# Kernel tuning notes

Hardware: AMD Instinct MI355X
Metric: run time of the kernel (lower is better)

The kernel has to match this reference:

```python
import jax, jax.numpy as jnp
import numpy as np
import math

B, M, DM = 8, 512, 1024
H, DH = 16, 64
DFF = 4096
RA, RF, RO = 32, 384, 384
EPS = 1e-12  # BERT LayerNorm eps


def layernorm(x, g, b):
    mu = jnp.mean(x, axis=-1, keepdims=True)
    var = jnp.mean(jnp.square(x - mu), axis=-1, keepdims=True)
    return (x - mu) * jax.lax.rsqrt(var + EPS) * g + b


def setup_inputs() -> dict:
    key = jax.random.key(0)
    ks = jax.random.split(key, 24)
    s = 0.02
    inp = {
        "x": jax.random.normal(ks[0], (B, M, DM), jnp.float32),
        "mask": jnp.zeros((B, M), jnp.float32),  # additive attention mask
        "Pq": jax.random.normal(ks[1], (H, DM, RA), jnp.float32) * s,
        "Vq": jax.random.normal(ks[2], (H, RA, DH), jnp.float32) * s,
        "Pk": jax.random.normal(ks[3], (H, DM, RA), jnp.float32) * s,
        "Vk": jax.random.normal(ks[4], (H, RA, DH), jnp.float32) * s,
        "Pv": jax.random.normal(ks[5], (H, DM, RA), jnp.float32) * s,
        "Vv": jax.random.normal(ks[6], (H, RA, DH), jnp.float32) * s,
        "bq": jax.random.normal(ks[7], (H, DH), jnp.float32) * s,
        "bk": jax.random.normal(ks[8], (H, DH), jnp.float32) * s,
        "bv": jax.random.normal(ks[9], (H, DH), jnp.float32) * s,
        "Uo": jax.random.normal(ks[10], (DM, RO), jnp.float32) * s,
        "Vo": jax.random.normal(ks[11], (RO, DM), jnp.float32) * s,
        "bo_attn": jax.random.normal(ks[12], (DM,), jnp.float32) * s,
        "U1": jax.random.normal(ks[13], (DM, RF), jnp.float32) * s,
        "V1": jax.random.normal(ks[14], (RF, DFF), jnp.float32) * s,
        "b1": jax.random.normal(ks[15], (DFF,), jnp.float32) * s,
        "U2": jax.random.normal(ks[16], (DFF, RF), jnp.float32) * s,
        "V2": jax.random.normal(ks[17], (RF, DM), jnp.float32) * s,
        "b2": jax.random.normal(ks[18], (DM,), jnp.float32) * s,
        "ln1_g": jnp.ones((DM,), jnp.float32),
        "ln1_b": jnp.zeros((DM,), jnp.float32),
        "ln2_g": jnp.ones((DM,), jnp.float32),
        "ln2_b": jnp.zeros((DM,), jnp.float32),
    }
    return inp


def reference(x, mask, Pq, Vq, Pk, Vk, Pv, Vv, bq, bk, bv,
              Uo, Vo, bo_attn, U1, V1, b1, U2, V2, b2,
              ln1_g, ln1_b, ln2_g, ln2_b):
    b_, m_, dm = x.shape
    h = Pq.shape[0]
    dh = dm // h
    # low-rank per-head projections: x -> [B,H,M,R] -> [B,H,M,dh]
    q = jnp.einsum('bmd,hdr->bhmr', x, Pq)
    k = jnp.einsum('bmd,hdr->bhmr', x, Pk)
    v = jnp.einsum('bmd,hdr->bhmr', x, Pv)
    Q = jnp.einsum('bhmr,hrd->bhmd', q, Vq) + bq[None, :, None, :]
    K = jnp.einsum('bhmr,hrd->bhmd', k, Vk) + bk[None, :, None, :]
    V = jnp.einsum('bhmr,hrd->bhmd', v, Vv) + bv[None, :, None, :]
    # scaled dot-product attention (flash_svd_attention equivalent)
    scores = jnp.einsum('bhmd,bhnd->bhmn', Q, K) / math.sqrt(dh)
    scores = scores + mask[:, None, None, :]
    probs = jax.nn.softmax(scores, axis=-1)
    attn = jnp.einsum('bhmn,bhnd->bhmd', probs, V)  # [B,H,M,dh]
    attn = attn.transpose(0, 2, 1, 3).reshape(b_, m_, dm)
    # low-rank output projection + residual + LN
    x1 = layernorm(x + (attn @ Uo) @ Vo + bo_attn, ln1_g, ln1_b)
    # flashsvd_ffn_v1 equivalent: gelu((x1 @ U1) @ V1 + b1) @ U2 @ V2 + b2
    mid = x1 @ U1
    hdn = jax.nn.gelu(mid @ V1 + b1, approximate=False)
    y = (hdn @ U2) @ V2 + b2
    out = layernorm(x1 + y, ln2_g, ln2_b)
    return out
```

## Files before the change

### kernel.cpp

```cpp
#include <hip/hip_runtime.h>
#include <math.h>

typedef __attribute__((ext_vector_type(8))) short short8;
typedef __attribute__((ext_vector_type(4))) float floatx4;

__device__ inline unsigned short f2bf(float f){
    union { float f; unsigned u; } v; v.f = f;
    unsigned r = v.u + 0x7fffu + ((v.u >> 16) & 1u);
    return (unsigned short)(r >> 16);
}
__device__ inline float bf2f(unsigned short b){
    union { unsigned u; float f; } v; v.u = ((unsigned)b) << 16;
    return v.f;
}
__device__ inline unsigned short to_bf(float f){ return f2bf(f); }
__device__ inline unsigned short to_bf(unsigned short u){ return u; }

#define GLD_LDS16(g, l) __builtin_amdgcn_global_load_lds( \
    (const __attribute__((address_space(1))) void*)(g),   \
    (__attribute__((address_space(3))) void*)(l), 16, 0, 0)

__global__ __launch_bounds__(256) void cast_kernel(const float* __restrict__ s,
                                                   unsigned short* __restrict__ d){
    int i = (blockIdx.x*256 + threadIdx.x)*4;
    float4 v = *(const float4*)(s+i);
    ushort4 o; o.x=f2bf(v.x); o.y=f2bf(v.y); o.z=f2bf(v.z); o.w=f2bf(v.w);
    *(ushort4*)(d+i) = o;
}

__global__ __launch_bounds__(256) void castP_kernel(
    const float* __restrict__ p0, const float* __restrict__ p1,
    const float* __restrict__ p2, unsigned short* __restrict__ d){
    int blk = blockIdx.x;
    int proj = blk >> 9;
    const float* s = (proj==0)?p0:(proj==1)?p1:p2;
    int off = (blk & 511)*1024 + threadIdx.x*4;
    float4 v = *(const float4*)(s+off);
    ushort4 o; o.x=f2bf(v.x); o.y=f2bf(v.y); o.z=f2bf(v.z); o.w=f2bf(v.w);
    *(ushort4*)(d + (size_t)proj*524288 + off) = o;
}

__global__ __launch_bounds__(256) void reduce4_kernel(
    const float* __restrict__ p, unsigned short* __restrict__ o, long mn){
    long i = ((long)blockIdx.x*256 + threadIdx.x)*4;
    float4 a = *(const float4*)(p+i);
    float4 b = *(const float4*)(p+mn+i);
    float4 c = *(const float4*)(p+2*mn+i);
    float4 d = *(const float4*)(p+3*mn+i);
    ushort4 r;
    r.x = f2bf(a.x+b.x+c.x+d.x); r.y = f2bf(a.y+b.y+c.y+d.y);
    r.z = f2bf(a.z+b.z+c.z+d.z); r.w = f2bf(a.w+b.w+c.w+d.w);
    *(ushort4*)(o+i) = r;
}

__global__ __launch_bounds__(256) void bcat_kernel(
    const float* __restrict__ bq, const float* __restrict__ bk,
    const float* __restrict__ bv, float* __restrict__ bcat){
    int i = blockIdx.x*256 + threadIdx.x;
    const float* p = (i < 1024) ? bq : (i < 2048) ? bk : bv;
    bcat[i] = p[i & 1023];
}

template<typename T>
__global__ __launch_bounds__(256) void trans_kernel(
    const T* __restrict__ src, unsigned short* __restrict__ dst,
    int R, int C, long sz, long dz)
{
    __shared__ unsigned short tile[32][33];
    const T* s = src + (size_t)blockIdx.z * sz;
    unsigned short* d = dst + (size_t)blockIdx.z * dz;
    int c0 = blockIdx.x*32, r0 = blockIdx.y*32;
    int tr = threadIdx.x>>3, tc = (threadIdx.x&7)*4;
    const T* sp = s + (size_t)(r0+tr)*C + c0 + tc;
#pragma unroll
    for (int i=0;i<4;i++) tile[tr][tc+i] = to_bf(sp[i]);
    __syncthreads();
    ushort4 o; o.x = tile[tc+0][tr]; o.y = tile[tc+1][tr];
    o.z = tile[tc+2][tr]; o.w = tile[tc+3][tr];
    *(ushort4*)(d + (size_t)(c0+tr)*R + r0 + tc) = o;
}

__global__ __launch_bounds__(256) void trans2_kernel(
    const float* __restrict__ s0, unsigned short* __restrict__ d0,
    const float* __restrict__ s1, unsigned short* __restrict__ d1,
    int R, int C)
{
    __shared__ unsigned short tile[32][33];
    const float* s = blockIdx.z ? s1 : s0;
    unsigned short* d = blockIdx.z ? d1 : d0;
    int c0 = blockIdx.x*32, r0 = blockIdx.y*32;
    int tr = threadIdx.x>>3, tc = (threadIdx.x&7)*4;
    const float* sp = s + (size_t)(r0+tr)*C + c0 + tc;
#pragma unroll
    for (int i=0;i<4;i++) tile[tr][tc+i] = f2bf(sp[i]);
    __syncthreads();
    ushort4 o; o.x = tile[tc+0][tr]; o.y = tile[tc+1][tr];
    o.z = tile[tc+2][tr]; o.w = tile[tc+3][tr];
    *(ushort4*)(d + (size_t)(c0+tr)*R + r0 + tc) = o;
}

__global__ __launch_bounds__(256) void vtrans3_kernel(
    const float* __restrict__ v0, const float* __restrict__ v1,
    const float* __restrict__ v2, unsigned short* __restrict__ dst)
{
    __shared__ unsigned short tile[32][33];
    int z = blockIdx.z;
    int proj = z >> 4, h = z & 15;
    const float* s = ((proj==0)?v0:(proj==1)?v1:v2) + h*2048;
    unsigned short* d = dst + (size_t)proj*32768 + h*2048;
    int c0 = blockIdx.x*32;
    int tr = threadIdx.x>>3, tc = (threadIdx.x&7)*4;
    const float* sp = s + (size_t)tr*64 + c0 + tc;
#pragma unroll
    for (int i=0;i<4;i++) tile[tr][tc+i] = f2bf(sp[i]);
    __syncthreads();
    ushort4 o; o.x = tile[tc+0][tr]; o.y = tile[tc+1][tr];
    o.z = tile[tc+2][tr]; o.w = tile[tc+3][tr];
    *(ushort4*)(d + (size_t)(c0+tr)*32 + tc) = o;
}

__global__ __launch_bounds__(256) void mm64_kernel(
    const unsigned short* __restrict__ A, const unsigned short* __restrict__ Bt,
    unsigned short* __restrict__ C, int Kdim, int lda, int ldb, int ldc,
    long ah, long al, long bh, long bl, long ch, long cl)
{
    __shared__ unsigned short As[64*40];
    __shared__ unsigned short Bs[64*40];
    int z = blockIdx.z;
    const unsigned short* Ab = A + (size_t)(z>>4)*ah + (size_t)(z&15)*al;
    const unsigned short* Bb = Bt + (size_t)(z>>4)*bh + (size_t)(z&15)*bl;
    int row0 = blockIdx.y*64, col0 = blockIdx.x*64;
    int t = threadIdx.x;
    int ar = t>>2, ak = (t&3)*8;
    int w = t>>6, lane = t&63, quad = lane>>4, c16 = lane&15;
    int wm = (w&1)*32, wn = (w>>1)*32;

    floatx4 zero = {0.f,0.f,0.f,0.f};
    floatx4 acc[2][2];
    acc[0][0]=zero; acc[0][1]=zero; acc[1][0]=zero; acc[1][1]=zero;

    const unsigned short* Ap = Ab + (size_t)(row0+ar)*lda + ak;
    const unsigned short* Bp = Bb + (size_t)(col0+ar)*ldb + ak;

    for (int kk=0; kk<Kdim; kk+=32){
        uint4 av = *(const uint4*)(Ap + kk);
        uint4 bv = *(const uint4*)(Bp + kk);
        __syncthreads();
        *(uint4*)(As + ar*40 + ak) = av;
        *(uint4*)(Bs + ar*40 + ak) = bv;
        __syncthreads();
        short8 a0 = *(const short8*)(As + (wm   +c16)*40 + quad*8);
        short8 a1 = *(const short8*)(As + (wm+16+c16)*40 + quad*8);
        short8 b0 = *(const short8*)(Bs + (wn   +c16)*40 + quad*8);
        short8 b1 = *(const short8*)(Bs + (wn+16+c16)*40 + quad*8);
        acc[0][0] = __builtin_amdgcn_mfma_f32_16x16x32_bf16(a0,b0,acc[0][0],0,0,0);
        acc[0][1] = __builtin_amdgcn_mfma_f32_16x16x32_bf16(a0,b1,acc[0][1],0,0,0);
        acc[1][0] = __builtin_amdgcn_mfma_f32_16x16x32_bf16(a1,b0,acc[1][0],0,0,0);
        acc[1][1] = __builtin_amdgcn_mfma_f32_16x16x32_bf16(a1,b1,acc[1][1],0,0,0);
    }

    size_t zc = (size_t)(z>>4)*ch + (size_t)(z&15)*cl;
#pragma unroll
    for (int mt=0; mt<2; mt++)
#pragma unroll
    for (int r=0; r<4; r++){
        int row = row0 + wm + mt*16 + quad*4 + r;
#pragma unroll
        for (int nt=0; nt<2; nt++){
            int col = col0 + wn + nt*16 + c16;
            C[zc + (size_t)row*ldc + col] = f2bf(acc[mt][nt][r]);
        }
    }
}

template<int EPI>
__global__ __launch_bounds__(256) void mm128_kernel(
    const unsigned short* __restrict__ A, const unsigned short* __restrict__ Bt,
    void* __restrict__ C, int Kdim, int lda, int ldb, int ldc,
    const float* __restrict__ aux, const float* __restrict__ resid)
{
    __shared__ unsigned short As[128*64];
    __shared__ unsigned short Bs[128*64];
    int row0 = blockIdx.y*128, col0 = blockIdx.x*128;
    int t = threadIdx.x;
    int w = t>>6, lane = t&63, quad = lane>>4, c16 = lane&15;
    int wm = (w&1)*64, wn = (w>>1)*64;

    int srow = lane>>3;
    int kc = (lane&7) ^ srow;
    const unsigned short* Ag = A + (size_t)(row0 + w*32 + srow)*lda + kc*8;
    const unsigned short* Bg = Bt + (size_t)(col0 + w*32 + srow)*ldb + kc*8;
    unsigned short* AsW = As + (w*32)*64;
    unsigned short* BsW = Bs + (w*32)*64;

    floatx4 acc[4][4];
#pragma unroll
    for (int i=0;i<4;i++)
#pragma unroll
    for (int j=0;j<4;j++) acc[i][j] = (floatx4){0.f,0.f,0.f,0.f};

    int xa = (c16&7)*8;

    for (int kk=0; kk<Kdim; kk+=64){
#pragma unroll
        for (int i=0;i<4;i++){
            GLD_LDS16(Ag + (size_t)(i*8)*lda + kk, AsW + i*512);
            GLD_LDS16(Bg + (size_t)(i*8)*ldb + kk, BsW + i*512);
        }
        __syncthreads();
#pragma unroll
        for (int ks=0; ks<2; ks++){
            short8 a[4], b[4];
#pragma unroll
            for (int mt=0; mt<4; mt++)
                a[mt] = *(const short8*)(As + (wm + mt*16 + c16)*64
                                            + (((ks*4 + quad)*8) ^ xa));
#pragma unroll
            for (int nt=0; nt<4; nt++)
                b[nt] = *(const short8*)(Bs + (wn + nt*16 + c16)*64
                                            + (((ks*4 + quad)*8) ^ xa));
#pragma unroll
            for (int mt=0; mt<4; mt++)
#pragma unroll
                for (int nt=0; nt<4; nt++)
                    acc[mt][nt] = __builtin_amdgcn_mfma_f32_16x16x32_bf16(
                        a[mt], b[nt], acc[mt][nt], 0,0,0);
        }
        __syncthreads();
    }

#pragma unroll
    for (int mt=0; mt<4; mt++)
#pragma unroll
    for (int r=0; r<4; r++){
        int row = row0 + wm + mt*16 + quad*4 + r;
#pragma unroll
        for (int nt=0; nt<4; nt++){
            int col = col0 + wn + nt*16 + c16;
            float v = acc[mt][nt][r];
            if (EPI==0) {
                ((unsigned short*)C)[(size_t)row*ldc + col] = f2bf(v);
            } else if (EPI==2) {
                v += aux[col];
                v = 0.5f*v*(1.0f + erff(v*0.70710678118654752f));
                ((unsigned short*)C)[(size_t)row*ldc + col] = f2bf(v);
            } else if (EPI==3) {
                ((float*)C)[(size_t)row*ldc + col] =
                    v + aux[col] + resid[(size_t)row*ldc + col];
            } else {
                int proj = col >> 10, cw = col & 1023;
                int b_ = row >> 9, m_ = row & 511;
                int hh = cw >> 6, dd = cw & 63;
                float vv = v + aux[col];
                if (proj == 0) vv *= 0.125f;
                size_t idx;
                if (proj == 2)
                    idx = (size_t)2*4194304 + ((size_t)(b_*16+hh)*64 + dd)*512 + m_;
                else
                    idx = (size_t)proj*4194304 + ((size_t)(b_*16+hh)*512 + m_)*64 + dd;
                ((unsigned short*)C)[idx] = f2bf(vv);
            }
        }
    }
}

__global__ __launch_bounds__(256) void mmsk_kernel(
    const unsigned short* __restrict__ A, const unsigned short* __restrict__ Bt,
    float* __restrict__ Cp, int Kchunk, int lda, int ldb, int ldc, long mn)
{
    __shared__ unsigned short As[128*64];
    __shared__ unsigned short Bs[128*64];
    int row0 = blockIdx.y*128, col0 = blockIdx.x*128;
    int t = threadIdx.x;
    int w = t>>6, lane = t&63, quad = lane>>4, c16 = lane&15;
    int wm = (w&1)*64, wn = (w>>1)*64;

    int srow = lane>>3;
    int kc = (lane&7) ^ srow;
    const unsigned short* Ag = A + (size_t)(row0 + w*32 + srow)*lda + kc*8;
    const unsigned short* Bg = Bt + (size_t)(col0 + w*32 + srow)*ldb + kc*8;
    unsigned short* AsW = As + (w*32)*64;
    unsigned short* BsW = Bs + (w*32)*64;

    floatx4 acc[4][4];
#pragma unroll
    for (int i=0;i<4;i++)
#pragma unroll
    for (int j=0;j<4;j++) acc[i][j] = (floatx4){0.f,0.f,0.f,0.f};

    int xa = (c16&7)*8;
    int k0 = blockIdx.z * Kchunk;
    for (int kk=k0; kk<k0+Kchunk; kk+=64){
#pragma unroll
        for (int i=0;i<4;i++){
            GLD_LDS16(Ag + (size_t)(i*8)*lda + kk, AsW + i*512);
            GLD_LDS16(Bg + (size_t)(i*8)*ldb + kk, BsW + i*512);
        }
        __syncthreads();
#pragma unroll
        for (int ks=0; ks<2; ks++){
            short8 a[4], b[4];
#pragma unroll
            for (int mt=0; mt<4; mt++)
                a[mt] = *(const short8*)(As + (wm + mt*16 + c16)*64
                                            + (((ks*4 + quad)*8) ^ xa));
#pragma unroll
            for (int nt=0; nt<4; nt++)
                b[nt] = *(const short8*)(Bs + (wn + nt*16 + c16)*64
                                            + (((ks*4 + quad)*8) ^ xa));
#pragma unroll
            for (int mt=0; mt<4; mt++)
#pragma unroll
                for (int nt=0; nt<4; nt++)
                    acc[mt][nt] = __builtin_amdgcn_mfma_f32_16x16x32_bf16(
                        a[mt], b[nt], acc[mt][nt], 0,0,0);
        }
        __syncthreads();
    }

    float* Cz = Cp + (size_t)blockIdx.z * mn;
#pragma unroll
    for (int mt=0; mt<4; mt++)
#pragma unroll
    for (int r=0; r<4; r++){
        int row = row0 + wm + mt*16 + quad*4 + r;
#pragma unroll
        for (int nt=0; nt<4; nt++){
            int col = col0 + wn + nt*16 + c16;
            Cz[(size_t)row*ldc + col] = acc[mt][nt][r];
        }
    }
}

__global__ __launch_bounds__(256) void flash_kernel(
    const unsigned short* __restrict__ Qb, const unsigned short* __restrict__ Kb,
    const unsigned short* __restrict__ Vt, const float* __restrict__ mask,
    unsigned short* __restrict__ attn)
{
    __shared__ unsigned short Ks[64*64];
    __shared__ unsigned short Vts[64*64];
    __shared__ unsigned short Ps[4][16*64];

    int qt = blockIdx.x, bh = blockIdx.y;
    int b = bh >> 4, h = bh & 15;
    int t = threadIdx.x;
    int w = t>>6, lane = t&63, quad = lane>>4, c16 = lane&15;

    int qrow = qt*64 + w*16 + c16;
    const unsigned short* Qp = Qb + ((size_t)bh*512 + qrow)*64 + quad*8;
    short8 qf0 = *(const short8*)(Qp);
    short8 qf1 = *(const short8*)(Qp + 32);

    const unsigned short* Ktile0 = Kb + (size_t)bh*512*64;
    const unsigned short* Vtbh = Vt + (size_t)bh*32768;

    int srow = lane>>3;
    int kc = (lane&7) ^ srow;
    int xa = (c16&7)*8;

    floatx4 Oacc[4];
#pragma unroll
    for (int nd=0;nd<4;nd++) Oacc[nd] = (floatx4){0.f,0.f,0.f,0.f};
    float mrow[4], lrow[4];
#pragma unroll
    for (int r=0;r<4;r++){ mrow[r] = -3.0e38f; lrow[r] = 0.f; }

    unsigned short* Pw = &Ps[w][0];

    for (int kt=0; kt<8; kt++){
        __syncthreads();
#pragma unroll
        for (int i=0;i<2;i++){
            GLD_LDS16(Ktile0 + (size_t)(kt*64 + w*16 + i*8 + srow)*64 + kc*8,
                      Ks + (w*16+i*8)*64);
            GLD_LDS16(Vtbh + (size_t)(w*16 + i*8 + srow)*512 + kt*64 + kc*8,
                      Vts + (w*16+i*8)*64);
        }
        __syncthreads();

        floatx4 Sacc[4];
#pragma unroll
        for (int nt=0;nt<4;nt++){
            float mv = mask[b*512 + kt*64 + nt*16 + c16];
            Sacc[nt] = (floatx4){mv,mv,mv,mv};
        }
#pragma unroll
        for (int ks=0; ks<2; ks++){
            short8 qk = ks ? qf1 : qf0;
            short8 bfr[4];
#pragma unroll
            for (int nt=0;nt<4;nt++)
                bfr[nt] = *(const short8*)(Ks + (nt*16 + c16)*64
                                              + (((ks*4 + quad)*8) ^ xa));
#pragma unroll
            for (int nt=0;nt<4;nt++)
                Sacc[nt] = __builtin_amdgcn_mfma_f32_16x16x32_bf16(
                    qk, bfr[nt], Sacc[nt], 0,0,0);
        }

#pragma unroll
        for (int r=0;r<4;r++){
            float sv0 = Sacc[0][r], sv1 = Sacc[1][r],
                  sv2 = Sacc[2][r], sv3 = Sacc[3][r];
            float rmax = fmaxf(fmaxf(sv0,sv1), fmaxf(sv2,sv3));
            rmax = fmaxf(rmax, __shfl_xor(rmax, 1));
            rmax = fmaxf(rmax, __shfl_xor(rmax, 2));
            rmax = fmaxf(rmax, __shfl_xor(rmax, 4));
            rmax = fmaxf(rmax, __shfl_xor(rmax, 8));
            float mold = mrow[r];
            float mnew = fmaxf(mold, rmax);
            float alpha = __expf(mold - mnew);
            float p0 = __expf(sv0-mnew), p1 = __expf(sv1-mnew);
            float p2 = __expf(sv2-mnew), p3 = __expf(sv3-mnew);
            float ps = p0+p1+p2+p3;
            ps += __shfl_xor(ps, 1);
            ps += __shfl_xor(ps, 2);
            ps += __shfl_xor(ps, 4);
            ps += __shfl_xor(ps, 8);
            lrow[r] = lrow[r]*alpha + ps;
            mrow[r] = mnew;
#pragma unroll
            for (int nd=0;nd<4;nd++) Oacc[nd][r] *= alpha;
            int rl = quad*4 + r;
            int rx = rl & 7;
            int cb = rl*64 + (c16&7);
            Pw[cb + (((0*2 + (c16>>3)) ^ rx)*8)] = f2bf(p0);
            Pw[cb + (((1*2 + (c16>>3)) ^ rx)*8)] = f2bf(p1);
            Pw[cb + (((2*2 + (c16>>3)) ^ rx)*8)] = f2bf(p2);
            Pw[cb + (((3*2 + (c16>>3)) ^ rx)*8)] = f2bf(p3);
        }

#pragma unroll
        for (int ks=0; ks<2; ks++){
            short8 pa = *(const short8*)(Pw + c16*64 + (((ks*4 + quad)*8) ^ xa));
            short8 bfr[4];
#pragma unroll
            for (int nd=0;nd<4;nd++)
                bfr[nd] = *(const short8*)(Vts + (nd*16 + c16)*64
                                               + (((ks*4 + quad)*8) ^ xa));
#pragma unroll
            for (int nd=0;nd<4;nd++)
                Oacc[nd] = __builtin_amdgcn_mfma_f32_16x16x32_bf16(
                    pa, bfr[nd], Oacc[nd], 0,0,0);
        }
    }

#pragma unroll
    for (int r=0;r<4;r++){
        int m = qt*64 + w*16 + quad*4 + r;
        float inv = 1.0f / lrow[r];
        unsigned short* op = attn + ((size_t)(b*512 + m))*1024 + h*64;
#pragma unroll
        for (int nd=0;nd<4;nd++)
            op[nd*16 + c16] = f2bf(Oacc[nd][r] * inv);
    }
}

template<int DUAL>
__global__ __launch_bounds__(256) void ln_kernel(
    const float* __restrict__ in, const float* __restrict__ g,
    const float* __restrict__ bta, float* __restrict__ outf,
    unsigned short* __restrict__ outb)
{
    int row = blockIdx.x;
    int t = threadIdx.x;
    const float* x = in + (size_t)row*1024;
    float4 xv = ((const float4*)x)[t];
    float s  = xv.x + xv.y + xv.z + xv.w;
    float ss = xv.x*xv.x + xv.y*xv.y + xv.z*xv.z + xv.w*xv.w;
#pragma unroll
    for (int off=32; off>0; off>>=1){ s += __shfl_down(s, off); ss += __shfl_down(ss, off); }
    __shared__ float rs[4], rss[4];
    int wid = t>>6, lane = t&63;
    if (lane==0){ rs[wid]=s; rss[wid]=ss; }
    __syncthreads();
    s  = rs[0]+rs[1]+rs[2]+rs[3];
    ss = rss[0]+rss[1]+rss[2]+rss[3];
    float mu  = s * (1.0f/1024.0f);
    float var = ss * (1.0f/1024.0f) - mu*mu;
    float inv = rsqrtf(var + 1e-12f);
    float4 gv = ((const float4*)g)[t];
    float4 bv = ((const float4*)bta)[t];
    float4 o = make_float4((xv.x-mu)*inv*gv.x+bv.x, (xv.y-mu)*inv*gv.y+bv.y,
                           (xv.z-mu)*inv*gv.z+bv.z, (xv.w-mu)*inv*gv.w+bv.w);
    ((float4*)(outf + (size_t)row*1024))[t] = o;
    if (DUAL){
        ushort4 ob; ob.x=f2bf(o.x); ob.y=f2bf(o.y); ob.z=f2bf(o.z); ob.w=f2bf(o.w);
        ((ushort4*)(outb + (size_t)row*1024))[t] = ob;
    }
}

extern "C" void kernel_launch(void* const* d_in, const int* in_sizes, int n_in,
                              void* d_out, int out_size, void* d_ws, size_t ws_size,
                              hipStream_t stream)
{
    const float* x       = (const float*)d_in[0];
    const float* mask    = (const float*)d_in[1];
    const float* Pq      = (const float*)d_in[2];
    const float* Vq      = (const float*)d_in[3];
    const float* Pk      = (const float*)d_in[4];
    const float* Vk      = (const float*)d_in[5];
    const float* Pv      = (const float*)d_in[6];
    const float* Vv      = (const float*)d_in[7];
    const float* bq      = (const float*)d_in[8];
    const float* bk      = (const float*)d_in[9];
    const float* bv      = (const float*)d_in[10];
    const float* Uo      = (const float*)d_in[11];
    const float* Vo      = (const float*)d_in[12];
    const float* bo_attn = (const float*)d_in[13];
    const float* U1      = (const float*)d_in[14];
    const float* V1      = (const float*)d_in[15];
    const float* b1      = (const float*)d_in[16];
    const float* U2      = (const float*)d_in[17];
    const float* V2      = (const float*)d_in[18];
    const float* b2      = (const float*)d_in[19];
    const float* ln1_g   = (const float*)d_in[20];
    const float* ln1_b   = (const float*)d_in[21];
    const float* ln2_g   = (const float*)d_in[22];
    const float* ln2_b   = (const float*)d_in[23];
    float* out = (float*)d_out;

    char* base = (char*)d_ws;
    unsigned short* Uo_t   = (unsigned short*)(base + 0);
    unsigned short* Vo_t   = (unsigned short*)(base + 786432);
    unsigned short* U1_t   = (unsigned short*)(base + 1572864);
    unsigned short* V1_t   = (unsigned short*)(base + 2359296);
    unsigned short* U2_t   = (unsigned short*)(base + 5505024);
    unsigned short* V2_t   = (unsigned short*)(base + 8650752);
    float*          bcat   = (float*)(base + 9437184);
    unsigned short* Wt     = (unsigned short*)(base + 9449472);
    unsigned short* Pbf    = (unsigned short*)(base + 15740928);
    unsigned short* Vt2    = (unsigned short*)(base + 18886656);
    unsigned short* x_bf   = (unsigned short*)(base + 19083264);
    unsigned short* t_bf   = (unsigned short*)(base + 9449472);
    float*          ybuf   = (float*)(base + 12595200);
    float*          x1     = (float*)(base + 29372416);
    unsigned short* x1_bf  = (unsigned short*)(base + 46149632);
    unsigned short* hdn_bf = (unsigned short*)(base + 54538240);
    float*          part0  = (float*)(base + 12595200);
    float*          part1  = (float*)(base + 54538240);
    float*          part2  = (float*)(base + 88092672);
    unsigned short* Qb     = (unsigned short*)(base + 76558336);
    unsigned short* Kb     = (unsigned short*)(base + 84946944);
    unsigned short* Vt     = (unsigned short*)(base + 93535552);
    unsigned short* attn_bf= (unsigned short*)(base + 110312768);

    const long MN384 = 4096L*384;

    cast_kernel<<<4096,256,0,stream>>>(x, x_bf);
    castP_kernel<<<1536,256,0,stream>>>(Pq, Pk, Pv, Pbf);
    vtrans3_kernel<<<dim3(2,1,48),256,0,stream>>>(Vq, Vk, Vv, Vt2);
    bcat_kernel<<<12,256,0,stream>>>(bq, bk, bv, bcat);
    trans2_kernel<<<dim3(12,32,2),256,0,stream>>>(Uo, Uo_t, U1, U1_t, 1024, 384);
    trans2_kernel<<<dim3(32,12,2),256,0,stream>>>(Vo, Vo_t, V2, V2_t, 384, 1024);
    trans_kernel<float><<<dim3(128,12,1),256,0,stream>>>(V1, V1_t, 384,4096, 0,0);
    trans_kernel<float><<<dim3(12,128,1),256,0,stream>>>(U2, U2_t, 4096,384, 0,0);

    mm64_kernel<<<dim3(16,1,48),256,0,stream>>>(Vt2, Pbf, Wt,
        32, 32, 32, 1024, 32768,2048, 524288,32768, 1048576,65536);

    mm128_kernel<4><<<dim3(24,32,1),256,0,stream>>>(x_bf, Wt, Qb,
        1024, 1024, 1024, 3072, bcat, nullptr);

    flash_kernel<<<dim3(8,128),256,0,stream>>>(Qb, Kb, Vt, mask, attn_bf);

    mmsk_kernel<<<dim3(3,32,4),256,0,stream>>>(attn_bf, Uo_t, part0,
        256, 1024, 1024, 384, MN384);
    reduce4_kernel<<<1536,256,0,stream>>>(part0, t_bf, MN384);
    mm128_kernel<3><<<dim3(8,32,1),256,0,stream>>>(t_bf, Vo_t, ybuf,
        384, 384, 384, 1024, bo_attn, x);
    ln_kernel<1><<<4096,256,0,stream>>>(ybuf, ln1_g, ln1_b, x1, x1_bf);
    mmsk_kernel<<<dim3(3,32,4),256,0,stream>>>(x1_bf, U1_t, part1,
        256, 1024, 1024, 384, MN384);
    reduce4_kernel<<<1536,256,0,stream>>>(part1, t_bf, MN384);
    mm128_kernel<2><<<dim3(32,32,1),256,0,stream>>>(t_bf, V1_t, hdn_bf,
        384, 384, 384, 4096, b1, nullptr);
    mmsk_kernel<<<dim3(3,32,4),256,0,stream>>>(hdn_bf, U2_t, part2,
        1024, 4096, 4096, 384, MN384);
    reduce4_kernel<<<1536,256,0,stream>>>(part2, t_bf, MN384);
    mm128_kernel<3><<<dim3(8,32,1),256,0,stream>>>(t_bf, V2_t, ybuf,
        384, 384, 384, 1024, b2, x1);
    ln_kernel<0><<<4096,256,0,stream>>>(ybuf, ln2_g, ln2_b, out, nullptr);
}
```

Baseline: 375.2 us.

## Merge prep kernels, stage GEMM epilogues through LDS, store split-K partials as bf16

Folds the eight weight and input cast/transpose launches into one prep kernel that dispatches on block index, cutting launch overhead. The GEMM epilogues (QKV scatter, GELU output, split-K partials) now stage the tile in shared memory and write 16-byte coalesced rows instead of scattered 2-byte stores. Split-K partials are stored as bf16 instead of fp32, halving partial traffic and reduce4 reads, at the cost of extra rounding before the sum.

```diff
diff --git a/kernel.cpp b/kernel.cpp
--- a/kernel.cpp
+++ b/kernel.cpp
@@ -13,83 +13,15 @@
     union { unsigned u; float f; } v; v.u = ((unsigned)b) << 16;
     return v.f;
 }
-__device__ inline unsigned short to_bf(float f){ return f2bf(f); }
-__device__ inline unsigned short to_bf(unsigned short u){ return u; }
 
 #define GLD_LDS16(g, l) __builtin_amdgcn_global_load_lds( \
     (const __attribute__((address_space(1))) void*)(g),   \
     (__attribute__((address_space(3))) void*)(l), 16, 0, 0)
 
-__global__ __launch_bounds__(256) void cast_kernel(const float* __restrict__ s,
-                                                   unsigned short* __restrict__ d){
-    int i = (blockIdx.x*256 + threadIdx.x)*4;
-    float4 v = *(const float4*)(s+i);
-    ushort4 o; o.x=f2bf(v.x); o.y=f2bf(v.y); o.z=f2bf(v.z); o.w=f2bf(v.w);
-    *(ushort4*)(d+i) = o;
-}
-
-__global__ __launch_bounds__(256) void castP_kernel(
-    const float* __restrict__ p0, const float* __restrict__ p1,
-    const float* __restrict__ p2, unsigned short* __restrict__ d){
-    int blk = blockIdx.x;
-    int proj = blk >> 9;
-    const float* s = (proj==0)?p0:(proj==1)?p1:p2;
-    int off = (blk & 511)*1024 + threadIdx.x*4;
-    float4 v = *(const float4*)(s+off);
-    ushort4 o; o.x=f2bf(v.x); o.y=f2bf(v.y); o.z=f2bf(v.z); o.w=f2bf(v.w);
-    *(ushort4*)(d + (size_t)proj*524288 + off) = o;
-}
-
-__global__ __launch_bounds__(256) void reduce4_kernel(
-    const float* __restrict__ p, unsigned short* __restrict__ o, long mn){
-    long i = ((long)blockIdx.x*256 + threadIdx.x)*4;
-    float4 a = *(const float4*)(p+i);
-    float4 b = *(const float4*)(p+mn+i);
-    float4 c = *(const float4*)(p+2*mn+i);
-    float4 d = *(const float4*)(p+3*mn+i);
-    ushort4 r;
-    r.x = f2bf(a.x+b.x+c.x+d.x); r.y = f2bf(a.y+b.y+c.y+d.y);
-    r.z = f2bf(a.z+b.z+c.z+d.z); r.w = f2bf(a.w+b.w+c.w+d.w);
-    *(ushort4*)(o+i) = r;
-}
-
-__global__ __launch_bounds__(256) void bcat_kernel(
-    const float* __restrict__ bq, const float* __restrict__ bk,
-    const float* __restrict__ bv, float* __restrict__ bcat){
-    int i = blockIdx.x*256 + threadIdx.x;
-    const float* p = (i < 1024) ? bq : (i < 2048) ? bk : bv;
-    bcat[i] = p[i & 1023];
-}
-
-template<typename T>
-__global__ __launch_bounds__(256) void trans_kernel(
-    const T* __restrict__ src, unsigned short* __restrict__ dst,
-    int R, int C, long sz, long dz)
-{
-    __shared__ unsigned short tile[32][33];
-    const T* s = src + (size_t)blockIdx.z * sz;
-    unsigned short* d = dst + (size_t)blockIdx.z * dz;
-    int c0 = blockIdx.x*32, r0 = blockIdx.y*32;
-    int tr = threadIdx.x>>3, tc = (threadIdx.x&7)*4;
-    const T* sp = s + (size_t)(r0+tr)*C + c0 + tc;
-#pragma unroll
-    for (int i=0;i<4;i++) tile[tr][tc+i] = to_bf(sp[i]);
-    __syncthreads();
-    ushort4 o; o.x = tile[tc+0][tr]; o.y = tile[tc+1][tr];
-    o.z = tile[tc+2][tr]; o.w = tile[tc+3][tr];
-    *(ushort4*)(d + (size_t)(c0+tr)*R + r0 + tc) = o;
-}
-
-__global__ __launch_bounds__(256) void trans2_kernel(
-    const float* __restrict__ s0, unsigned short* __restrict__ d0,
-    const float* __restrict__ s1, unsigned short* __restrict__ d1,
-    int R, int C)
-{
-    __shared__ unsigned short tile[32][33];
-    const float* s = blockIdx.z ? s1 : s0;
-    unsigned short* d = blockIdx.z ? d1 : d0;
-    int c0 = blockIdx.x*32, r0 = blockIdx.y*32;
-    int tr = threadIdx.x>>3, tc = (threadIdx.x&7)*4;
+__device__ inline void tbody(const float* __restrict__ s,
+                             unsigned short* __restrict__ d, int R, int C,
+                             int c0, int r0, int t, unsigned short tile[][33]){
+    int tr = t>>3, tc = (t&7)*4;
     const float* sp = s + (size_t)(r0+tr)*C + c0 + tc;
 #pragma unroll
     for (int i=0;i<4;i++) tile[tr][tc+i] = f2bf(sp[i]);
@@ -99,24 +31,90 @@
     *(ushort4*)(d + (size_t)(c0+tr)*R + r0 + tc) = o;
 }
 
-__global__ __launch_bounds__(256) void vtrans3_kernel(
-    const float* __restrict__ v0, const float* __restrict__ v1,
-    const float* __restrict__ v2, unsigned short* __restrict__ dst)
+__global__ __launch_bounds__(256) void prep_kernel(
+    const float* __restrict__ x, unsigned short* __restrict__ x_bf,
+    const float* __restrict__ Pq, const float* __restrict__ Pk,
+    const float* __restrict__ Pv, unsigned short* __restrict__ Pbf,
+    const float* __restrict__ Vq, const float* __restrict__ Vk,
+    const float* __restrict__ Vv, unsigned short* __restrict__ Vt2,
+    const float* __restrict__ bq, const float* __restrict__ bk,
+    const float* __restrict__ bv, float* __restrict__ bcat,
+    const float* __restrict__ Uo, unsigned short* __restrict__ Uo_t,
+    const float* __restrict__ U1, unsigned short* __restrict__ U1_t,
+    const float* __restrict__ Vo, unsigned short* __restrict__ Vo_t,
+    const float* __restrict__ V2, unsigned short* __restrict__ V2_t,
+    const float* __restrict__ V1, unsigned short* __restrict__ V1_t,
+    const float* __restrict__ U2, unsigned short* __restrict__ U2_t)
 {
     __shared__ unsigned short tile[32][33];
-    int z = blockIdx.z;
-    int proj = z >> 4, h = z & 15;
-    const float* s = ((proj==0)?v0:(proj==1)?v1:v2) + h*2048;
-    unsigned short* d = dst + (size_t)proj*32768 + h*2048;
-    int c0 = blockIdx.x*32;
-    int tr = threadIdx.x>>3, tc = (threadIdx.x&7)*4;
-    const float* sp = s + (size_t)tr*64 + c0 + tc;
-#pragma unroll
-    for (int i=0;i<4;i++) tile[tr][tc+i] = f2bf(sp[i]);
-    __syncthreads();
-    ushort4 o; o.x = tile[tc+0][tr]; o.y = tile[tc+1][tr];
-    o.z = tile[tc+2][tr]; o.w = tile[tc+3][tr];
-    *(ushort4*)(d + (size_t)(c0+tr)*32 + tc) = o;
+    int bid = blockIdx.x, t = threadIdx.x;
+    if (bid < 4096){
+        int i = (bid*256 + t)*4;
+        float4 v = *(const float4*)(x+i);
+        ushort4 o; o.x=f2bf(v.x); o.y=f2bf(v.y); o.z=f2bf(v.z); o.w=f2bf(v.w);
+        *(ushort4*)(x_bf+i) = o;
+    } else if (bid < 5632){
+        int blk = bid - 4096;
+        int proj = blk >> 9;
+        const float* s = (proj==0)?Pq:(proj==1)?Pk:Pv;
+        int off = (blk & 511)*1024 + t*4;
+        float4 v = *(const float4*)(s+off);
+        ushort4 o; o.x=f2bf(v.x); o.y=f2bf(v.y); o.z=f2bf(v.z); o.w=f2bf(v.w);
+        *(ushort4*)(Pbf + (size_t)proj*524288 + off) = o;
+    } else if (bid < 5728){
+        int local = bid - 5632;
+        int gx = local & 1, z = local >> 1;
+        int proj = z >> 4, h = z & 15;
+        const float* s = ((proj==0)?Vq:(proj==1)?Vk:Vv) + h*2048;
+        unsigned short* d = Vt2 + (size_t)proj*32768 + h*2048;
+        int c0 = gx*32;
+        int tr = t>>3, tc = (t&7)*4;
+        const float* sp = s + (size_t)tr*64 + c0 + tc;
+#pragma unroll
+        for (int i=0;i<4;i++) tile[tr][tc+i] = f2bf(sp[i]);
+        __syncthreads();
+        ushort4 o; o.x = tile[tc+0][tr]; o.y = tile[tc+1][tr];
+        o.z = tile[tc+2][tr]; o.w = tile[tc+3][tr];
+        *(ushort4*)(d + (size_t)(c0+tr)*32 + tc) = o;
+    } else if (bid < 5740){
+        int i = (bid-5728)*256 + t;
+        const float* p = (i < 1024) ? bq : (i < 2048) ? bk : bv;
+        bcat[i] = p[i & 1023];
+    } else if (bid < 6508){
+        int local = bid - 5740;
+        const float* s = Uo; unsigned short* d = Uo_t;
+        if (local >= 384){ s = U1; d = U1_t; local -= 384; }
+        tbody(s, d, 1024, 384, (local%12)*32, (local/12)*32, t, tile);
+    } else if (bid < 7276){
+        int local = bid - 6508;
+        const float* s = Vo; unsigned short* d = Vo_t;
+        if (local >= 384){ s = V2; d = V2_t; local -= 384; }
+        tbody(s, d, 384, 1024, (local%32)*32, (local/32)*32, t, tile);
+    } else if (bid < 8812){
+        int local = bid - 7276;
+        tbody(V1, V1_t, 384, 4096, (local%128)*32, (local/128)*32, t, tile);
+    } else {
+        int local = bid - 8812;
+        tbody(U2, U2_t, 4096, 384, (local%12)*32, (local/12)*32, t, tile);
+    }
+}
+
+__global__ __launch_bounds__(256) void reduce4_kernel(
+    const unsigned short* __restrict__ p, unsigned short* __restrict__ o, long mn){
+    long i = ((long)blockIdx.x*256 + threadIdx.x)*8;
+    uint4 a = *(const uint4*)(p+i);
+    uint4 b = *(const uint4*)(p+mn+i);
+    uint4 c = *(const uint4*)(p+2*mn+i);
+    uint4 d = *(const uint4*)(p+3*mn+i);
+    const unsigned short* ua = (const unsigned short*)&a;
+    const unsigned short* ub = (const unsigned short*)&b;
+    const unsigned short* uc = (const unsigned short*)&c;
+    const unsigned short* ud = (const unsigned short*)&d;
+    uint4 r; unsigned short* ur = (unsigned short*)&r;
+#pragma unroll
+    for (int j=0;j<8;j++)
+        ur[j] = f2bf(bf2f(ua[j]) + bf2f(ub[j]) + bf2f(uc[j]) + bf2f(ud[j]));
+    *(uint4*)(o+i) = r;
 }
 
 __global__ __launch_bounds__(256) void mm64_kernel(
@@ -179,8 +177,9 @@
     void* __restrict__ C, int Kdim, int lda, int ldb, int ldc,
     const float* __restrict__ aux, const float* __restrict__ resid)
 {
-    __shared__ unsigned short As[128*64];
-    __shared__ unsigned short Bs[128*64];
+    __shared__ unsigned short smem[(EPI==3) ? 16384 : 17408];
+    unsigned short* As = smem;
+    unsigned short* Bs = smem + 8192;
     int row0 = blockIdx.y*128, col0 = blockIdx.x*128;
     int t = threadIdx.x;
     int w = t>>6, lane = t&63, quad = lane>>4, c16 = lane&15;
@@ -229,47 +228,76 @@
         __syncthreads();
     }
 
+    if (EPI==3){
+#pragma unroll
+        for (int mt=0; mt<4; mt++)
+#pragma unroll
+        for (int r=0; r<4; r++){
+            int row = row0 + wm + mt*16 + quad*4 + r;
+#pragma unroll
+            for (int nt=0; nt<4; nt++){
+                int col = col0 + wn + nt*16 + c16;
+                ((float*)C)[(size_t)row*ldc + col] =
+                    acc[mt][nt][r] + aux[col] + resid[(size_t)row*ldc + col];
+            }
+        }
+        return;
+    }
+
+    int proj = col0 >> 10;
 #pragma unroll
     for (int mt=0; mt<4; mt++)
 #pragma unroll
     for (int r=0; r<4; r++){
-        int row = row0 + wm + mt*16 + quad*4 + r;
+        int row_l = wm + mt*16 + quad*4 + r;
 #pragma unroll
         for (int nt=0; nt<4; nt++){
-            int col = col0 + wn + nt*16 + c16;
+            int col_l = wn + nt*16 + c16;
             float v = acc[mt][nt][r];
-            if (EPI==0) {
-                ((unsigned short*)C)[(size_t)row*ldc + col] = f2bf(v);
-            } else if (EPI==2) {
-                v += aux[col];
+            if (EPI==2){
+                v += aux[col0 + col_l];
                 v = 0.5f*v*(1.0f + erff(v*0.70710678118654752f));
-                ((unsigned short*)C)[(size_t)row*ldc + col] = f2bf(v);
-            } else if (EPI==3) {
-                ((float*)C)[(size_t)row*ldc + col] =
-                    v + aux[col] + resid[(size_t)row*ldc + col];
+                smem[row_l*136 + col_l] = f2bf(v);
             } else {
-                int proj = col >> 10, cw = col & 1023;
-                int b_ = row >> 9, m_ = row & 511;
-                int hh = cw >> 6, dd = cw & 63;
-                float vv = v + aux[col];
-                if (proj == 0) vv *= 0.125f;
-                size_t idx;
-                if (proj == 2)
-                    idx = (size_t)2*4194304 + ((size_t)(b_*16+hh)*64 + dd)*512 + m_;
-                else
-                    idx = (size_t)proj*4194304 + ((size_t)(b_*16+hh)*512 + m_)*64 + dd;
-                ((unsigned short*)C)[idx] = f2bf(vv);
+                v += aux[col0 + col_l];
+                if (proj == 0) v *= 0.125f;
+                if (proj < 2) smem[row_l*136 + col_l] = f2bf(v);
+                else          smem[col_l*136 + row_l] = f2bf(v);
             }
         }
+    }
+    __syncthreads();
+    int b_ = row0 >> 9;
+    int m0 = row0 & 511;
+    int cbase = col0 & 1023;
+#pragma unroll
+    for (int i=0;i<8;i++){
+        int rr = i*16 + (t>>4);
+        int cc = (t&15)*8;
+        uint4 val = *(const uint4*)(smem + rr*136 + cc);
+        unsigned short* dst;
+        if (EPI==2){
+            dst = (unsigned short*)C + (size_t)(row0+rr)*ldc + col0 + cc;
+        } else if (proj < 2){
+            int cw = cbase + cc; int hh = cw>>6, dd = cw&63;
+            dst = (unsigned short*)C + (size_t)proj*4194304
+                + ((size_t)(b_*16+hh)*512 + m0 + rr)*64 + dd;
+        } else {
+            int cw = cbase + rr; int hh = cw>>6, dd = cw&63;
+            dst = (unsigned short*)C + (size_t)2*4194304
+                + ((size_t)(b_*16+hh)*64 + dd)*512 + m0 + cc;
+        }
+        *(uint4*)dst = val;
     }
 }
 
 __global__ __launch_bounds__(256) void mmsk_kernel(
     const unsigned short* __restrict__ A, const unsigned short* __restrict__ Bt,
-    float* __restrict__ Cp, int Kchunk, int lda, int ldb, int ldc, long mn)
+    unsigned short* __restrict__ Cp, int Kchunk, int lda, int ldb, int ldc, long mn)
 {
-    __shared__ unsigned short As[128*64];
-    __shared__ unsigned short Bs[128*64];
+    __shared__ unsigned short smem[17408];
+    unsigned short* As = smem;
+    unsigned short* Bs = smem + 8192;
     int row0 = blockIdx.y*128, col0 = blockIdx.x*128;
     int t = threadIdx.x;
     int w = t>>6, lane = t&63, quad = lane>>4, c16 = lane&15;
@@ -318,17 +346,25 @@
         __syncthreads();
     }
 
-    float* Cz = Cp + (size_t)blockIdx.z * mn;
 #pragma unroll
     for (int mt=0; mt<4; mt++)
 #pragma unroll
     for (int r=0; r<4; r++){
-        int row = row0 + wm + mt*16 + quad*4 + r;
+        int row_l = wm + mt*16 + quad*4 + r;
 #pragma unroll
         for (int nt=0; nt<4; nt++){
-            int col = col0 + wn + nt*16 + c16;
-            Cz[(size_t)row*ldc + col] = acc[mt][nt][r];
-        }
+            int col_l = wn + nt*16 + c16;
+            smem[row_l*136 + col_l] = f2bf(acc[mt][nt][r]);
+        }
+    }
+    __syncthreads();
+    unsigned short* Cz = Cp + (size_t)blockIdx.z * mn;
+#pragma unroll
+    for (int i=0;i<8;i++){
+        int rr = i*16 + (t>>4);
+        int cc = (t&15)*8;
+        uint4 val = *(const uint4*)(smem + rr*136 + cc);
+        *(uint4*)(Cz + (size_t)(row0+rr)*ldc + col0 + cc) = val;
     }
 }
 
@@ -537,9 +573,9 @@
     float*          x1     = (float*)(base + 29372416);
     unsigned short* x1_bf  = (unsigned short*)(base + 46149632);
     unsigned short* hdn_bf = (unsigned short*)(base + 54538240);
-    float*          part0  = (float*)(base + 12595200);
-    float*          part1  = (float*)(base + 54538240);
-    float*          part2  = (float*)(base + 88092672);
+    unsigned short* part0  = (unsigned short*)(base + 12595200);
+    unsigned short* part1  = (unsigned short*)(base + 54538240);
+    unsigned short* part2  = (unsigned short*)(base + 88092672);
     unsigned short* Qb     = (unsigned short*)(base + 76558336);
     unsigned short* Kb     = (unsigned short*)(base + 84946944);
     unsigned short* Vt     = (unsigned short*)(base + 93535552);
@@ -547,14 +583,9 @@
 
     const long MN384 = 4096L*384;
 
-    cast_kernel<<<4096,256,0,stream>>>(x, x_bf);
-    castP_kernel<<<1536,256,0,stream>>>(Pq, Pk, Pv, Pbf);
-    vtrans3_kernel<<<dim3(2,1,48),256,0,stream>>>(Vq, Vk, Vv, Vt2);
-    bcat_kernel<<<12,256,0,stream>>>(bq, bk, bv, bcat);
-    trans2_kernel<<<dim3(12,32,2),256,0,stream>>>(Uo, Uo_t, U1, U1_t, 1024, 384);
-    trans2_kernel<<<dim3(32,12,2),256,0,stream>>>(Vo, Vo_t, V2, V2_t, 384, 1024);
-    trans_kernel<float><<<dim3(128,12,1),256,0,stream>>>(V1, V1_t, 384,4096, 0,0);
-    trans_kernel<float><<<dim3(12,128,1),256,0,stream>>>(U2, U2_t, 4096,384, 0,0);
+    prep_kernel<<<10348,256,0,stream>>>(x, x_bf, Pq, Pk, Pv, Pbf,
+        Vq, Vk, Vv, Vt2, bq, bk, bv, bcat,
+        Uo, Uo_t, U1, U1_t, Vo, Vo_t, V2, V2_t, V1, V1_t, U2, U2_t);
 
     mm64_kernel<<<dim3(16,1,48),256,0,stream>>>(Vt2, Pbf, Wt,
         32, 32, 32, 1024, 32768,2048, 524288,32768, 1048576,65536);
@@ -566,18 +597,18 @@
 
     mmsk_kernel<<<dim3(3,32,4),256,0,stream>>>(attn_bf, Uo_t, part0,
         256, 1024, 1024, 384, MN384);
-    reduce4_kernel<<<1536,256,0,stream>>>(part0, t_bf, MN384);
+    reduce4_kernel<<<768,256,0,stream>>>(part0, t_bf, MN384);
     mm128_kernel<3><<<dim3(8,32,1),256,0,stream>>>(t_bf, Vo_t, ybuf,
         384, 384, 384, 1024, bo_attn, x);
     ln_kernel<1><<<4096,256,0,stream>>>(ybuf, ln1_g, ln1_b, x1, x1_bf);
     mmsk_kernel<<<dim3(3,32,4),256,0,stream>>>(x1_bf, U1_t, part1,
         256, 1024, 1024, 384, MN384);
-    reduce4_kernel<<<1536,256,0,stream>>>(part1, t_bf, MN384);
+    reduce4_kernel<<<768,256,0,stream>>>(part1, t_bf, MN384);
     mm128_kernel<2><<<dim3(32,32,1),256,0,stream>>>(t_bf, V1_t, hdn_bf,
         384, 384, 384, 4096, b1, nullptr);
     mmsk_kernel<<<dim3(3,32,4),256,0,stream>>>(hdn_bf, U2_t, part2,
         1024, 4096, 4096, 384, MN384);
-    reduce4_kernel<<<1536,256,0,stream>>>(part2, t_bf, MN384);
+    reduce4_kernel<<<768,256,0,stream>>>(part2, t_bf, MN384);
     mm128_kernel<3><<<dim3(8,32,1),256,0,stream>>>(t_bf, V2_t, ybuf,
         384, 384, 384, 1024, b2, x1);
     ln_kernel<0><<<4096,256,0,stream>>>(ybuf, ln2_g, ln2_b, out, nullptr);
```

Result: faster. 335.9 us (-10.5%).
